# Performance work log

Measured on AMD Instinct MI355X. Metric: run time of the kernel, lower is better.

The kernel has to match this reference:

```python
import jax, jax.numpy as jnp
import numpy as np

N_NODES = 100000
N_EDGES = 3200000
IN_DIM, HID, OUT_DIM = 512, 64, 5


def _glorot(key, shape):
    fan_in, fan_out = shape[0], shape[1]
    lim = np.sqrt(6.0 / (fan_in + fan_out))
    return jax.random.uniform(key, shape, jnp.float32, -lim, lim)


def setup_inputs() -> dict:
    key = jax.random.key(0)
    ks = jax.random.split(key, 10)
    x = jax.random.normal(ks[0], (N_NODES, IN_DIM), jnp.float32)
    edge_index = jax.random.randint(ks[1], (2, N_EDGES), 0, N_NODES, jnp.int64)
    edge_weight = jax.random.uniform(ks[2], (N_EDGES,), jnp.float32)
    return {
        "x": x,
        "edge_index": edge_index,
        "edge_weight": edge_weight,
        "W1": _glorot(ks[3], (IN_DIM, HID)),
        "b1": jnp.zeros((HID,), jnp.float32),
        "W2": _glorot(ks[4], (HID, HID)),
        "b2": jnp.zeros((HID,), jnp.float32),
        "Wfc": _glorot(ks[5], (HID, OUT_DIM)),
        "bfc": jnp.zeros((OUT_DIM,), jnp.float32),
    }


def _gcn_norm(edge_index, edge_weight, num_nodes):
    # PyG gcn_norm: add self-loops (weight 1), symmetric deg^-1/2 normalization.
    loop = jnp.arange(num_nodes, dtype=edge_index.dtype)
    src = jnp.concatenate([edge_index[0], loop])
    dst = jnp.concatenate([edge_index[1], loop])
    ew = jnp.concatenate([edge_weight, jnp.ones((num_nodes,), edge_weight.dtype)])
    deg = jax.ops.segment_sum(ew, dst, num_segments=num_nodes)
    dinv = jnp.where(deg > 0, jax.lax.rsqrt(deg), 0.0)
    norm = dinv[src] * ew * dinv[dst]
    return src, dst, norm


def _gcn_conv(x, W, b, src, dst, norm, num_nodes):
    h = x @ W  # transform first (GCNConv does lin before propagate)
    msg = norm[:, None] * h[src]  # gather + scale  [E, d]
    out = jax.ops.segment_sum(msg, dst, num_segments=num_nodes)  # scatter-add
    return out + b


def reference(x, edge_index, edge_weight, W1, b1, W2, b2, Wfc, bfc):
    n = x.shape[0]
    src, dst, norm = _gcn_norm(edge_index, edge_weight, n)
    h = jax.nn.relu(_gcn_conv(x, W1, b1, src, dst, norm, n))
    h = jax.nn.relu(_gcn_conv(h, W2, b2, src, dst, norm, n))
    return h @ Wfc + bfc
```

## Files before the change

kernel.cpp:

```cpp
#include <hip/hip_runtime.h>

#define IN_DIM 512
#define HID 64
#define OUT_DIM 5


__device__ __forceinline__ unsigned short f2bf(float f) {
    unsigned u = __float_as_uint(f);
    u += 0x7FFF + ((u >> 16) & 1);
    return (unsigned short)(u >> 16);
}
__device__ __forceinline__ float bf2f(unsigned short b) {
    return __uint_as_float(((unsigned)b) << 16);
}


__global__ void k_init(unsigned long long* __restrict__ packed, int n) {
    int i = blockIdx.x * blockDim.x + threadIdx.x;
    if (i < n) packed[i] = 0ULL;
}


__global__ void k_hist(const int* __restrict__ dst, const float* __restrict__ ew,
                       unsigned long long* __restrict__ packed, int* __restrict__ rank, int nE) {
    int e = blockIdx.x * blockDim.x + threadIdx.x;
    if (e < nE) {
        int d = dst[e];
        unsigned long long fx = (unsigned long long)(ew[e] * 4294967296.0);
        unsigned long long old = atomicAdd(&packed[d], (1ULL << 44) | fx);
        rank[e] = (int)(old >> 44);
    }
}


__global__ void k_dinv(const unsigned long long* __restrict__ packed,
                       float* __restrict__ dinv, int* __restrict__ cnt, int n) {
    int i = blockIdx.x * blockDim.x + threadIdx.x;
    if (i < n) {
        unsigned long long p = packed[i];
        int c = (int)(p >> 44);
        double ewsum = (double)(p & ((1ULL << 44) - 1)) * (1.0 / 4294967296.0);
        float deg = 1.0f + (float)ewsum;
        dinv[i] = rsqrtf(deg);
        cnt[i] = c;
    }
}


__global__ void k_scan1(const int* __restrict__ cnt, int* __restrict__ rowptr,
                        int* __restrict__ bsum, int n) {
    __shared__ int sdata[256];
    int t = threadIdx.x, b = blockIdx.x;
    int base = b * 1024 + t * 4;
    int v[4], s = 0;
#pragma unroll
    for (int k = 0; k < 4; ++k) { int i = base + k; v[k] = (i < n) ? cnt[i] : 0; s += v[k]; }
    sdata[t] = s;
    __syncthreads();
    int x = s;
    for (int off = 1; off < 256; off <<= 1) {
        int y = (t >= off) ? sdata[t - off] : 0;
        __syncthreads();
        x += y;
        sdata[t] = x;
        __syncthreads();
    }
    int run = x - s;
    if (t == 255) bsum[b] = x;
#pragma unroll
    for (int k = 0; k < 4; ++k) { int i = base + k; if (i < n) rowptr[i] = run; run += v[k]; }
}

__global__ void k_scan2(int* __restrict__ bsum, int nb) {
    __shared__ int sdata[256];
    int t = threadIdx.x;
    int s = (t < nb) ? bsum[t] : 0;
    sdata[t] = s;
    __syncthreads();
    int x = s;
    for (int off = 1; off < 256; off <<= 1) {
        int y = (t >= off) ? sdata[t - off] : 0;
        __syncthreads();
        x += y;
        sdata[t] = x;
        __syncthreads();
    }
    if (t < nb) bsum[t] = x - s;
}

__global__ void k_scan3(int* __restrict__ rowptr, const int* __restrict__ bsum, int n, int E) {
    int i = blockIdx.x * blockDim.x + threadIdx.x;
    if (i < n) rowptr[i] += bsum[i >> 10];
    else if (i == n) rowptr[n] = E;
}


__global__ void k_reorder(const int* __restrict__ src, const int* __restrict__ dst,
                          const float* __restrict__ ew, const float* __restrict__ dinv,
                          const int* __restrict__ rowptr, const int* __restrict__ rank,
                          int2* __restrict__ edges, int nE) {
    int e = blockIdx.x * blockDim.x + threadIdx.x;
    if (e < nE) {
        int s = src[e];
        int d = dst[e];
        float w = dinv[s] * ew[e] * dinv[d];
        int pos = rowptr[d] + rank[e];
        edges[pos] = make_int2(s, __float_as_int(w));
    }
}


__launch_bounds__(256)
__global__ void k_aggregate(const float* __restrict__ h, const unsigned short* __restrict__ hb,
                            const float* __restrict__ dinv,
                            const int2* __restrict__ edges, const int* __restrict__ rowptr,
                            float* __restrict__ out, int N) {
    int n = (blockIdx.x * 256 + threadIdx.x) >> 6;
    int lane = threadIdx.x & 63;
    if (n >= N) return;

    float dn = dinv[n];
    float acc = dn * dn * h[(size_t)n * HID + lane];

    int beg = rowptr[n], end = rowptr[n + 1];
    int j = beg;
    for (; j + 3 < end; j += 4) {
        int2 p0 = edges[j];
        int2 p1 = edges[j + 1];
        int2 p2 = edges[j + 2];
        int2 p3 = edges[j + 3];
        float h0 = bf2f(hb[(size_t)p0.x * HID + lane]);
        float h1 = bf2f(hb[(size_t)p1.x * HID + lane]);
        float h2 = bf2f(hb[(size_t)p2.x * HID + lane]);
        float h3 = bf2f(hb[(size_t)p3.x * HID + lane]);
        acc = fmaf(__int_as_float(p0.y), h0, acc);
        acc = fmaf(__int_as_float(p1.y), h1, acc);
        acc = fmaf(__int_as_float(p2.y), h2, acc);
        acc = fmaf(__int_as_float(p3.y), h3, acc);
    }
    for (; j < end; ++j) {
        int2 p = edges[j];
        acc = fmaf(__int_as_float(p.y), bf2f(hb[(size_t)p.x * HID + lane]), acc);
    }
    out[(size_t)n * HID + lane] = acc;
}


template <int K_, bool RELU_BIAS>
__launch_bounds__(256)
__global__ void k_gemm_n64(const float* __restrict__ A, const float* __restrict__ W,
                           const float* __restrict__ bias, float* __restrict__ out,
                           unsigned short* __restrict__ outb, int M) {
    constexpr int BK = 16;
    __shared__ float As[BK][68];
    __shared__ float Ws[BK][64];

    const int t  = threadIdx.x;
    const int tx = t & 15;
    const int ty = t >> 4;
    const int row0 = blockIdx.x * 64;

    const int lr = t >> 2;
    const int lk = (t & 3) * 4;

    float acc[4][4] = {};

    for (int k0 = 0; k0 < K_; k0 += BK) {
        float4 av = make_float4(0.f, 0.f, 0.f, 0.f);
        int ar = row0 + lr;
        if (ar < M) {
            av = *(const float4*)&A[(long long)ar * K_ + k0 + lk];
            if (RELU_BIAS) {
                const float4 bv = *(const float4*)&bias[k0 + lk];
                av.x = fmaxf(av.x + bv.x, 0.f);
                av.y = fmaxf(av.y + bv.y, 0.f);
                av.z = fmaxf(av.z + bv.z, 0.f);
                av.w = fmaxf(av.w + bv.w, 0.f);
            }
        }
        As[lk + 0][lr] = av.x;
        As[lk + 1][lr] = av.y;
        As[lk + 2][lr] = av.z;
        As[lk + 3][lr] = av.w;

        *(float4*)&Ws[t >> 4][(t & 15) * 4] =
            *(const float4*)&W[(long long)(k0 + (t >> 4)) * 64 + (t & 15) * 4];

        __syncthreads();

#pragma unroll
        for (int kk = 0; kk < BK; ++kk) {
            float4 a4 = *(const float4*)&As[kk][ty * 4];
            float4 b4 = *(const float4*)&Ws[kk][tx * 4];
            float a[4] = {a4.x, a4.y, a4.z, a4.w};
            float b[4] = {b4.x, b4.y, b4.z, b4.w};
#pragma unroll
            for (int i = 0; i < 4; ++i)
#pragma unroll
                for (int j = 0; j < 4; ++j)
                    acc[i][j] = fmaf(a[i], b[j], acc[i][j]);
        }
        __syncthreads();
    }

#pragma unroll
    for (int i = 0; i < 4; ++i) {
        int r = row0 + ty * 4 + i;
        if (r < M) {
            *(float4*)&out[(long long)r * 64 + tx * 4] =
                make_float4(acc[i][0], acc[i][1], acc[i][2], acc[i][3]);
            ushort4 hv;
            hv.x = f2bf(acc[i][0]);
            hv.y = f2bf(acc[i][1]);
            hv.z = f2bf(acc[i][2]);
            hv.w = f2bf(acc[i][3]);
            *(ushort4*)&outb[(long long)r * 64 + tx * 4] = hv;
        }
    }
}


__launch_bounds__(256)
__global__ void k_final(const float* __restrict__ agg, const float* __restrict__ b2,
                        const float* __restrict__ Wfc, const float* __restrict__ bfc,
                        float* __restrict__ out, int N) {
    __shared__ float Wsf[HID * OUT_DIM];
    __shared__ float bs[HID];
    int t = threadIdx.x;
    for (int i = t; i < HID * OUT_DIM; i += 256) Wsf[i] = Wfc[i];
    if (t < HID) bs[t] = b2[t];
    __syncthreads();

    int n = blockIdx.x * blockDim.x + t;
    if (n >= N) return;

    float acc[OUT_DIM];
#pragma unroll
    for (int o = 0; o < OUT_DIM; ++o) acc[o] = bfc[o];

    const float4* ag = (const float4*)&agg[(long long)n * HID];
#pragma unroll
    for (int k4 = 0; k4 < HID / 4; ++k4) {
        float4 v4 = ag[k4];
        float v[4] = {v4.x, v4.y, v4.z, v4.w};
#pragma unroll
        for (int j = 0; j < 4; ++j) {
            int k = k4 * 4 + j;
            float f = fmaxf(v[j] + bs[k], 0.f);
#pragma unroll
            for (int o = 0; o < OUT_DIM; ++o)
                acc[o] = fmaf(f, Wsf[k * OUT_DIM + o], acc[o]);
        }
    }
#pragma unroll
    for (int o = 0; o < OUT_DIM; ++o) out[(long long)n * OUT_DIM + o] = acc[o];
}


static inline size_t align_up(size_t x, size_t a) { return (x + a - 1) & ~(a - 1); }

extern "C" void kernel_launch(void* const* d_in, const int* in_sizes, int n_in,
                              void* d_out, int out_size, void* d_ws, size_t ws_size,
                              hipStream_t stream) {
    const float* x   = (const float*)d_in[0];
    const int*   ei  = (const int*)d_in[1];
    const float* ew  = (const float*)d_in[2];
    const float* W1  = (const float*)d_in[3];
    const float* b1  = (const float*)d_in[4];
    const float* W2  = (const float*)d_in[5];
    const float* b2  = (const float*)d_in[6];
    const float* Wfc = (const float*)d_in[7];
    const float* bfc = (const float*)d_in[8];
    float* out = (float*)d_out;

    const int E = in_sizes[2];
    const int N = in_sizes[0] / IN_DIM;
    const int* src = ei;
    const int* dst = ei + E;

    char* p = (char*)d_ws;
    unsigned long long* packed = (unsigned long long*)p; p += align_up((size_t)N * 8, 256);
    float* dinv   = (float*)p;  p += align_up((size_t)N * 4, 256);
    int*   cnt    = (int*)p;    p += align_up((size_t)N * 4, 256);
    int*   rowptr = (int*)p;    p += align_up((size_t)(N + 1) * 4, 256);
    int*   bsum   = (int*)p;    p += align_up((size_t)256 * 4, 256);
    int*   rank   = (int*)p;    p += align_up((size_t)E * 4, 256);
    unsigned short* hb = (unsigned short*)rank;
    int2*  edges  = (int2*)p;   p += align_up((size_t)E * 8, 256);
    float* bufA   = (float*)p;  p += align_up((size_t)N * HID * 4, 256);
    float* bufB   = (float*)p;  p += align_up((size_t)N * HID * 4, 256);
    (void)ws_size; (void)n_in; (void)out_size;

    const int BS = 256;
    dim3 blk(BS);
    int gN  = (N + BS - 1) / BS;
    int gN1 = (N + 1 + BS - 1) / BS;
    int gE  = (E + BS - 1) / BS;
    int gM  = (N + 63) / 64;
    int nb  = (N + 1023) / 1024;
    int gAg = (N + 3) / 4;

    k_init<<<gN, blk, 0, stream>>>(packed, N);
    k_hist<<<gE, blk, 0, stream>>>(dst, ew, packed, rank, E);
    k_dinv<<<gN, blk, 0, stream>>>(packed, dinv, cnt, N);
    k_scan1<<<nb, blk, 0, stream>>>(cnt, rowptr, bsum, N);
    k_scan2<<<1, blk, 0, stream>>>(bsum, nb);
    k_scan3<<<gN1, blk, 0, stream>>>(rowptr, bsum, N, E);
    k_reorder<<<gE, blk, 0, stream>>>(src, dst, ew, dinv, rowptr, rank, edges, E);

    k_gemm_n64<IN_DIM, false><<<gM, blk, 0, stream>>>(x, W1, nullptr, bufA, hb, N);
    k_aggregate<<<gAg, blk, 0, stream>>>(bufA, hb, dinv, edges, rowptr, bufB, N);

    k_gemm_n64<HID, true><<<gM, blk, 0, stream>>>(bufB, W2, b1, bufA, hb, N);
    k_aggregate<<<gAg, blk, 0, stream>>>(bufA, hb, dinv, edges, rowptr, bufB, N);

    k_final<<<gN, blk, 0, stream>>>(bufB, b2, Wfc, bfc, out, N);
}
```

Measured before the change: 840.3 us.

## Split aggregation into 16-feature quarter slabs with feature-major bf16 layout

The bf16 feature table is stored as four 16-column slabs ([q][N][16]), and aggregation runs one grid row per slab. Inside a slab, each wave splits a node's edges over four 16-lane slots and combines them with cross-lane shuffles. Each slab is smaller, so gathers should hit cache more often, though every edge list is now read four times. The histogram kernel is also vectorized to four edges per thread, and the GEMM and final kernels are adapted to the slab layout.

```diff
diff --git a/kernel.cpp b/kernel.cpp
--- a/kernel.cpp
+++ b/kernel.cpp
@@ -14,6 +14,9 @@
     return __uint_as_float(((unsigned)b) << 16);
 }
 
+__device__ __forceinline__ int ed_src(long long v) { return (int)(v & 0xffffffffLL); }
+__device__ __forceinline__ float ed_w(long long v) { return __int_as_float((int)(v >> 32)); }
+
 
 __global__ void k_init(unsigned long long* __restrict__ packed, int n) {
     int i = blockIdx.x * blockDim.x + threadIdx.x;
@@ -21,14 +24,33 @@
 }
 
 
-__global__ void k_hist(const int* __restrict__ dst, const float* __restrict__ ew,
-                       unsigned long long* __restrict__ packed, int* __restrict__ rank, int nE) {
-    int e = blockIdx.x * blockDim.x + threadIdx.x;
-    if (e < nE) {
-        int d = dst[e];
-        unsigned long long fx = (unsigned long long)(ew[e] * 4294967296.0);
-        unsigned long long old = atomicAdd(&packed[d], (1ULL << 44) | fx);
-        rank[e] = (int)(old >> 44);
+__global__ void k_hist4(const int* __restrict__ dst, const float* __restrict__ ew,
+                        unsigned long long* __restrict__ packed, int* __restrict__ rank, int nE) {
+    int base = (blockIdx.x * blockDim.x + threadIdx.x) * 4;
+    if (base + 3 < nE) {
+        int4   d4 = *(const int4*)&dst[base];
+        float4 w4 = *(const float4*)&ew[base];
+        unsigned long long f0 = (unsigned long long)(w4.x * 4294967296.0);
+        unsigned long long f1 = (unsigned long long)(w4.y * 4294967296.0);
+        unsigned long long f2 = (unsigned long long)(w4.z * 4294967296.0);
+        unsigned long long f3 = (unsigned long long)(w4.w * 4294967296.0);
+        unsigned long long o0 = atomicAdd(&packed[d4.x], (1ULL << 44) | f0);
+        unsigned long long o1 = atomicAdd(&packed[d4.y], (1ULL << 44) | f1);
+        unsigned long long o2 = atomicAdd(&packed[d4.z], (1ULL << 44) | f2);
+        unsigned long long o3 = atomicAdd(&packed[d4.w], (1ULL << 44) | f3);
+        int4 r4;
+        r4.x = (int)(o0 >> 44);
+        r4.y = (int)(o1 >> 44);
+        r4.z = (int)(o2 >> 44);
+        r4.w = (int)(o3 >> 44);
+        *(int4*)&rank[base] = r4;
+    } else {
+        for (int e = base; e < nE; ++e) {
+            int d = dst[e];
+            unsigned long long fx = (unsigned long long)(ew[e] * 4294967296.0);
+            unsigned long long old = atomicAdd(&packed[d], (1ULL << 44) | fx);
+            rank[e] = (int)(old >> 44);
+        }
     }
 }
 
@@ -111,42 +133,51 @@
 
 
 __launch_bounds__(256)
-__global__ void k_aggregate(const float* __restrict__ h, const unsigned short* __restrict__ hb,
-                            const float* __restrict__ dinv,
-                            const int2* __restrict__ edges, const int* __restrict__ rowptr,
-                            float* __restrict__ out, int N) {
-    int n = (blockIdx.x * 256 + threadIdx.x) >> 6;
-    int lane = threadIdx.x & 63;
+__global__ void k_aggregate_q(const float* __restrict__ h,
+                              const unsigned short* __restrict__ hbq,
+                              const float* __restrict__ dinv,
+                              const int2* __restrict__ edges, const int* __restrict__ rowptr,
+                              float* __restrict__ outq,
+                              int N) {
+    const int q    = blockIdx.y;
+    const int wave = threadIdx.x >> 6;
+    const int n    = blockIdx.x * 4 + wave;
     if (n >= N) return;
-
-    float dn = dinv[n];
-    float acc = dn * dn * h[(size_t)n * HID + lane];
-
-    int beg = rowptr[n], end = rowptr[n + 1];
-    int j = beg;
-    for (; j + 3 < end; j += 4) {
-        int2 p0 = edges[j];
-        int2 p1 = edges[j + 1];
-        int2 p2 = edges[j + 2];
-        int2 p3 = edges[j + 3];
-        float h0 = bf2f(hb[(size_t)p0.x * HID + lane]);
-        float h1 = bf2f(hb[(size_t)p1.x * HID + lane]);
-        float h2 = bf2f(hb[(size_t)p2.x * HID + lane]);
-        float h3 = bf2f(hb[(size_t)p3.x * HID + lane]);
-        acc = fmaf(__int_as_float(p0.y), h0, acc);
-        acc = fmaf(__int_as_float(p1.y), h1, acc);
-        acc = fmaf(__int_as_float(p2.y), h2, acc);
-        acc = fmaf(__int_as_float(p3.y), h3, acc);
-    }
-    for (; j < end; ++j) {
-        int2 p = edges[j];
-        acc = fmaf(__int_as_float(p.y), bf2f(hb[(size_t)p.x * HID + lane]), acc);
-    }
-    out[(size_t)n * HID + lane] = acc;
-}
-
-
-template <int K_, bool RELU_BIAS>
+    const int lane = threadIdx.x & 63;
+    const int slot = lane >> 4;
+    const int f    = lane & 15;
+
+    const unsigned short* __restrict__ hq = hbq + (size_t)q * N * 16;
+    const long long* __restrict__ edg = (const long long*)edges;
+
+    float dn  = dinv[n];
+    float acc = 0.f;
+    if (slot == 0) acc = dn * dn * h[(size_t)n * 64 + q * 16 + f];
+
+    const int beg = rowptr[n], end = rowptr[n + 1];
+    int j = beg + slot;
+    for (; j + 4 < end; j += 8) {
+        long long p0 = __builtin_nontemporal_load(&edg[j]);
+        long long p1 = __builtin_nontemporal_load(&edg[j + 4]);
+        float h0 = bf2f(hq[(size_t)ed_src(p0) * 16 + f]);
+        float h1 = bf2f(hq[(size_t)ed_src(p1) * 16 + f]);
+        acc = fmaf(ed_w(p0), h0, acc);
+        acc = fmaf(ed_w(p1), h1, acc);
+    }
+    if (j < end) {
+        long long p = __builtin_nontemporal_load(&edg[j]);
+        acc = fmaf(ed_w(p), bf2f(hq[(size_t)ed_src(p) * 16 + f]), acc);
+    }
+
+    acc += __shfl_xor(acc, 16, 64);
+    acc += __shfl_xor(acc, 32, 64);
+
+    if (slot == 0)
+        __builtin_nontemporal_store(acc, &outq[((size_t)q * N + n) * 16 + f]);
+}
+
+
+template <int K_, bool RELU_BIAS, bool QMAJOR_A>
 __launch_bounds__(256)
 __global__ void k_gemm_n64(const float* __restrict__ A, const float* __restrict__ W,
                            const float* __restrict__ bias, float* __restrict__ out,
@@ -169,7 +200,10 @@
         float4 av = make_float4(0.f, 0.f, 0.f, 0.f);
         int ar = row0 + lr;
         if (ar < M) {
-            av = *(const float4*)&A[(long long)ar * K_ + k0 + lk];
+            const float* ap = QMAJOR_A
+                ? &A[((size_t)(k0 >> 4) * M + ar) * 16 + lk]
+                : &A[(long long)ar * K_ + k0 + lk];
+            av = *(const float4*)ap;
             if (RELU_BIAS) {
                 const float4 bv = *(const float4*)&bias[k0 + lk];
                 av.x = fmaxf(av.x + bv.x, 0.f);
@@ -203,6 +237,8 @@
         __syncthreads();
     }
 
+    const int colq = (tx * 4) >> 4;
+    const int colf = (tx * 4) & 15;
 #pragma unroll
     for (int i = 0; i < 4; ++i) {
         int r = row0 + ty * 4 + i;
@@ -214,7 +250,7 @@
             hv.y = f2bf(acc[i][1]);
             hv.z = f2bf(acc[i][2]);
             hv.w = f2bf(acc[i][3]);
-            *(ushort4*)&outb[(long long)r * 64 + tx * 4] = hv;
+            *(ushort4*)&outb[((size_t)colq * M + r) * 16 + colf] = hv;
         }
     }
 }
@@ -238,18 +274,21 @@
 #pragma unroll
     for (int o = 0; o < OUT_DIM; ++o) acc[o] = bfc[o];
 
-    const float4* ag = (const float4*)&agg[(long long)n * HID];
-#pragma unroll
-    for (int k4 = 0; k4 < HID / 4; ++k4) {
-        float4 v4 = ag[k4];
-        float v[4] = {v4.x, v4.y, v4.z, v4.w};
-#pragma unroll
-        for (int j = 0; j < 4; ++j) {
-            int k = k4 * 4 + j;
-            float f = fmaxf(v[j] + bs[k], 0.f);
-#pragma unroll
-            for (int o = 0; o < OUT_DIM; ++o)
-                acc[o] = fmaf(f, Wsf[k * OUT_DIM + o], acc[o]);
+#pragma unroll
+    for (int q = 0; q < 4; ++q) {
+        const float4* ag = (const float4*)&agg[((size_t)q * N + n) * 16];
+#pragma unroll
+        for (int k4 = 0; k4 < 4; ++k4) {
+            float4 v4 = ag[k4];
+            float v[4] = {v4.x, v4.y, v4.z, v4.w};
+#pragma unroll
+            for (int j = 0; j < 4; ++j) {
+                int k = q * 16 + k4 * 4 + j;
+                float f = fmaxf(v[j] + bs[k], 0.f);
+#pragma unroll
+                for (int o = 0; o < OUT_DIM; ++o)
+                    acc[o] = fmaf(f, Wsf[k * OUT_DIM + o], acc[o]);
+            }
         }
     }
 #pragma unroll
@@ -285,7 +324,7 @@
     int*   rowptr = (int*)p;    p += align_up((size_t)(N + 1) * 4, 256);
     int*   bsum   = (int*)p;    p += align_up((size_t)256 * 4, 256);
     int*   rank   = (int*)p;    p += align_up((size_t)E * 4, 256);
-    unsigned short* hb = (unsigned short*)rank;
+    unsigned short* hbq = (unsigned short*)rank;
     int2*  edges  = (int2*)p;   p += align_up((size_t)E * 8, 256);
     float* bufA   = (float*)p;  p += align_up((size_t)N * HID * 4, 256);
     float* bufB   = (float*)p;  p += align_up((size_t)N * HID * 4, 256);
@@ -296,23 +335,24 @@
     int gN  = (N + BS - 1) / BS;
     int gN1 = (N + 1 + BS - 1) / BS;
     int gE  = (E + BS - 1) / BS;
+    int gE4 = (E + BS * 4 - 1) / (BS * 4);
     int gM  = (N + 63) / 64;
     int nb  = (N + 1023) / 1024;
-    int gAg = (N + 3) / 4;
+    dim3 gAgg((N + 3) / 4, 4);
 
     k_init<<<gN, blk, 0, stream>>>(packed, N);
-    k_hist<<<gE, blk, 0, stream>>>(dst, ew, packed, rank, E);
+    k_hist4<<<gE4, blk, 0, stream>>>(dst, ew, packed, rank, E);
     k_dinv<<<gN, blk, 0, stream>>>(packed, dinv, cnt, N);
     k_scan1<<<nb, blk, 0, stream>>>(cnt, rowptr, bsum, N);
     k_scan2<<<1, blk, 0, stream>>>(bsum, nb);
     k_scan3<<<gN1, blk, 0, stream>>>(rowptr, bsum, N, E);
     k_reorder<<<gE, blk, 0, stream>>>(src, dst, ew, dinv, rowptr, rank, edges, E);
 
-    k_gemm_n64<IN_DIM, false><<<gM, blk, 0, stream>>>(x, W1, nullptr, bufA, hb, N);
-    k_aggregate<<<gAg, blk, 0, stream>>>(bufA, hb, dinv, edges, rowptr, bufB, N);
-
-    k_gemm_n64<HID, true><<<gM, blk, 0, stream>>>(bufB, W2, b1, bufA, hb, N);
-    k_aggregate<<<gAg, blk, 0, stream>>>(bufA, hb, dinv, edges, rowptr, bufB, N);
+    k_gemm_n64<IN_DIM, false, false><<<gM, blk, 0, stream>>>(x, W1, nullptr, bufA, hbq, N);
+    k_aggregate_q<<<gAgg, blk, 0, stream>>>(bufA, hbq, dinv, edges, rowptr, bufB, N);
+
+    k_gemm_n64<HID, true, true><<<gM, blk, 0, stream>>>(bufB, W2, b1, bufA, hbq, N);
+    k_aggregate_q<<<gAgg, blk, 0, stream>>>(bufA, hbq, dinv, edges, rowptr, bufB, N);
 
     k_final<<<gN, blk, 0, stream>>>(bufB, b2, Wfc, bfc, out, N);
 }
```

Result: slower. 1.211 ms (+44.1%).
